# Performance work log

Measured on AMD Instinct MI355X. Metric: run time of the kernel, lower is better.

## Reference

```python
import jax, jax.numpy as jnp
import numpy as np

B, N, F = 8, 1024, 512
H, D = 4, 128  # num_heads, output_dim
LEAKY_ALPHA = 0.2
MASK_VAL = -1e10


def setup_inputs() -> dict:
    key = jax.random.key(0)
    ks = jax.random.split(key, 6)
    X = jax.random.normal(ks[0], (B, N, F), dtype=jnp.float32)
    A = (jax.random.uniform(ks[1], (B, N, N)) < 0.05).astype(jnp.float32)
    A = jnp.maximum(A, jnp.eye(N, dtype=jnp.float32)[None])
    W_att = jax.random.normal(ks[2], (H, F, D), dtype=jnp.float32) * (1.0 / np.sqrt(F))
    a_att = jax.random.normal(ks[3], (H, 2, D), dtype=jnp.float32) * (1.0 / np.sqrt(D))
    kernel = jax.random.normal(ks[4], (H, F, D), dtype=jnp.float32) * (1.0 / np.sqrt(F))
    bias = jax.random.normal(ks[5], (H * D,), dtype=jnp.float32) * 0.02
    return {"X": X, "A": A, "W_att": W_att, "a_att": a_att, "kernel": kernel, "bias": bias}


def reference(X, A, W_att, a_att, kernel, bias):
    # Per-head feature projection used only for attention scores: [H,B,N,D]
    xf = jnp.einsum('bnf,hfd->hbnd', X, W_att)
    att_self = jnp.einsum('hbnd,hd->hbn', xf, a_att[:, 0])       # [H,B,N]
    att_neigh = jnp.einsum('hbnd,hd->hbn', xf, a_att[:, 1])      # [H,B,N]
    # additive scores: scores[h,b,i,j] = self[i] + neigh[j]
    scores = att_self[..., :, None] + att_neigh[..., None, :]    # [H,B,N,N]
    scores = jnp.where(scores >= 0, scores, LEAKY_ALPHA * scores)
    scores = scores + MASK_VAL * (1.0 - A)[None]                 # adjacency mask
    attn = jax.nn.softmax(scores, axis=-1)                       # [H,B,N,N]
    # aggregate raw features X, then per-head kernel projection
    agg = jnp.einsum('hbij,bjf->hbif', attn, X)                  # [H,B,N,F]
    out = jnp.einsum('hbnf,hfd->bnhd', agg, kernel)              # [B,N,H,D]
    out = out.reshape(out.shape[0], out.shape[1], -1)            # concat heads -> [B,N,H*D]
    out = out + bias
    return jax.nn.elu(out)
```

## Files before the change

kernel.cpp:

```cpp
#include <hip/hip_runtime.h>
#include <hip/hip_bf16.h>
#include <math.h>

namespace {
constexpr int B = 8, N = 1024, F = 512, H = 4, D = 128, HD = H * D;
constexpr int ROWS = B * N;
constexpr float LEAKY = 0.2f;

constexpr size_t UV_OFF  = 0;
constexpr size_t ATT_OFF = 4096;
constexpr size_t Y_OFF   = 69632;
constexpr size_t XB_OFF  = 2166784;
constexpr size_t WKB_OFF = 4263936;
}

typedef __attribute__((ext_vector_type(8))) short short8;
typedef __attribute__((ext_vector_type(4))) float f32x4;

__device__ __forceinline__ ushort bf16bits(float x) {
    __hip_bfloat16 h = __float2bfloat16(x);
    return *reinterpret_cast<ushort*>(&h);
}
__device__ __forceinline__ float blo(uint u) {
    return __uint_as_float(u << 16);
}
__device__ __forceinline__ float bhi(uint u) {
    return __uint_as_float(u & 0xffff0000u);
}

extern "C" __global__ __launch_bounds__(256) void k_pre(
    const float* __restrict__ Watt, const float* __restrict__ aatt,
    const float* __restrict__ Wk, float* __restrict__ uv,
    __hip_bfloat16* __restrict__ Wkb) {
    __shared__ ushort T[128][136];
    if (blockIdx.x < 16) {
        int h = blockIdx.x >> 2, f0 = (blockIdx.x & 3) * 128;
#pragma unroll
        for (int p = 0; p < 16; ++p) {
            int fi = p * 8 + (threadIdx.x >> 5);
            int d4 = (threadIdx.x & 31) * 4;
            float4 v = *reinterpret_cast<const float4*>(
                Wk + ((size_t)h * F + f0 + fi) * D + d4);
            T[d4 + 0][fi] = bf16bits(v.x);
            T[d4 + 1][fi] = bf16bits(v.y);
            T[d4 + 2][fi] = bf16bits(v.z);
            T[d4 + 3][fi] = bf16bits(v.w);
        }
        __syncthreads();
        int d = threadIdx.x >> 1, hf = threadIdx.x & 1;
        ushort* dst =
            (ushort*)Wkb + (size_t)(h * 128 + d) * F + f0 + hf * 64;
        const ushort* src = &T[d][hf * 64];
#pragma unroll
        for (int q = 0; q < 8; ++q)
            *reinterpret_cast<uint4*>(dst + q * 8) =
                *reinterpret_cast<const uint4*>(src + q * 8);
    } else {
        int t = (blockIdx.x - 16) * 256 + threadIdx.x;
        int f = t % F;
        int h = (t / F) % H;
        int w = t / (F * H);
        const float* Wrow = Watt + (size_t)(h * F + f) * D;
        const float* arow = aatt + (size_t)(h * 2 + w) * D;
        float s = 0.f;
#pragma unroll 4
        for (int d = 0; d < D; ++d) s = fmaf(Wrow[d], arow[d], s);
        uv[(size_t)w * (H * F) + h * F + f] = s;
    }
}

extern "C" __global__ __launch_bounds__(256) void k_att(
    const float* __restrict__ X, const float* __restrict__ uv,
    float* __restrict__ att, __hip_bfloat16* __restrict__ Xb) {
    int wave = threadIdx.x >> 6, lane = threadIdx.x & 63;
    int row = blockIdx.x * 4 + wave;
    const float4* xr = reinterpret_cast<const float4*>(X + (size_t)row * F);
    float4 v0 = xr[lane * 2], v1 = xr[lane * 2 + 1];

    union { short8 s; ushort u[8]; } pk;
    pk.u[0] = bf16bits(v0.x); pk.u[1] = bf16bits(v0.y);
    pk.u[2] = bf16bits(v0.z); pk.u[3] = bf16bits(v0.w);
    pk.u[4] = bf16bits(v1.x); pk.u[5] = bf16bits(v1.y);
    pk.u[6] = bf16bits(v1.z); pk.u[7] = bf16bits(v1.w);
    *reinterpret_cast<short8*>(Xb + (size_t)row * F + lane * 8) = pk.s;

    float acc[2][H];
#pragma unroll
    for (int w = 0; w < 2; ++w)
#pragma unroll
        for (int h = 0; h < H; ++h) {
            const float4* up = reinterpret_cast<const float4*>(
                uv + (size_t)w * (H * F) + h * F + lane * 8);
            float4 u0 = up[0], u1 = up[1];
            float a = 0.f;
            a = fmaf(v0.x, u0.x, a); a = fmaf(v0.y, u0.y, a);
            a = fmaf(v0.z, u0.z, a); a = fmaf(v0.w, u0.w, a);
            a = fmaf(v1.x, u1.x, a); a = fmaf(v1.y, u1.y, a);
            a = fmaf(v1.z, u1.z, a); a = fmaf(v1.w, u1.w, a);
            acc[w][h] = a;
        }
#pragma unroll
    for (int w = 0; w < 2; ++w)
#pragma unroll
        for (int h = 0; h < H; ++h) {
            float v = acc[w][h];
#pragma unroll
            for (int off = 32; off > 0; off >>= 1) v += __shfl_xor(v, off);
            if (lane == 0) att[(size_t)w * (H * ROWS) + h * ROWS + row] = v;
        }
}

extern "C" __global__ __launch_bounds__(256) void k_gemm(
    const __hip_bfloat16* __restrict__ Xb,
    const __hip_bfloat16* __restrict__ Wkb,
    __hip_bfloat16* __restrict__ Y) {
    __shared__ __align__(16) char smem[24576];
    int tid = threadIdx.x;
    int lane = tid & 63, wv = tid >> 6;
    int wr = wv >> 1, wc = wv & 1;
    int lt = (blockIdx.x & 7) * 64 + (blockIdx.x >> 3);
    int bm = lt >> 3, bn = lt & 7;
    int row0 = bm * 128, col0 = bn * 64;

    const ushort* Ag = (const ushort*)Xb;
    const ushort* Bg = (const ushort*)Wkb;

    int aoff[4][2], boff[2][2];
#pragma unroll
    for (int ks = 0; ks < 2; ++ks) {
        int cb = ks * 4 + (lane >> 4);
#pragma unroll
        for (int mi = 0; mi < 4; ++mi) {
            int ra = wr * 64 + mi * 16 + (lane & 15);
            aoff[mi][ks] = ra * 128 + (cb ^ (ra & 7)) * 16;
        }
#pragma unroll
        for (int ni = 0; ni < 2; ++ni) {
            int rb = wc * 32 + ni * 16 + (lane & 15);
            boff[ni][ks] = 16384 + rb * 128 + (cb ^ (rb & 7)) * 16;
        }
    }
    int srowA[4], sgbA[4], srowB[2], sgbB[2];
#pragma unroll
    for (int i = 0; i < 4; ++i) {
        srowA[i] = i * 32 + wv * 8 + (lane >> 3);
        sgbA[i] = (lane & 7) ^ (srowA[i] & 7);
    }
#pragma unroll
    for (int i = 0; i < 2; ++i) {
        srowB[i] = i * 32 + wv * 8 + (lane >> 3);
        sgbB[i] = (lane & 7) ^ (srowB[i] & 7);
    }

    f32x4 acc[4][2] = {};
    for (int k0 = 0; k0 < F; k0 += 64) {
        __syncthreads();
#pragma unroll
        for (int i = 0; i < 4; ++i) {
            const ushort* ga = Ag + (size_t)(row0 + srowA[i]) * F + k0 + sgbA[i] * 8;
            __builtin_amdgcn_global_load_lds(
                (const __attribute__((address_space(1))) uint32_t*)ga,
                (__attribute__((address_space(3))) uint32_t*)(smem + i * 4096 + wv * 1024),
                16, 0, 0);
        }
#pragma unroll
        for (int i = 0; i < 2; ++i) {
            const ushort* gb = Bg + (size_t)(col0 + srowB[i]) * F + k0 + sgbB[i] * 8;
            __builtin_amdgcn_global_load_lds(
                (const __attribute__((address_space(1))) uint32_t*)gb,
                (__attribute__((address_space(3))) uint32_t*)(smem + 16384 + i * 4096 + wv * 1024),
                16, 0, 0);
        }
        __syncthreads();
#pragma unroll
        for (int ks = 0; ks < 2; ++ks) {
            short8 af[4], bf[2];
#pragma unroll
            for (int mi = 0; mi < 4; ++mi)
                af[mi] = *reinterpret_cast<short8*>(smem + aoff[mi][ks]);
#pragma unroll
            for (int ni = 0; ni < 2; ++ni)
                bf[ni] = *reinterpret_cast<short8*>(smem + boff[ni][ks]);
#pragma unroll
            for (int mi = 0; mi < 4; ++mi)
#pragma unroll
                for (int ni = 0; ni < 2; ++ni)
                    acc[mi][ni] = __builtin_amdgcn_mfma_f32_16x16x32_bf16(
                        af[mi], bf[ni], acc[mi][ni], 0, 0, 0);
        }
    }
    int cr = (lane >> 4) * 4, cc = lane & 15;
#pragma unroll
    for (int mi = 0; mi < 4; ++mi)
#pragma unroll
        for (int ni = 0; ni < 2; ++ni) {
            int gr = row0 + wr * 64 + mi * 16 + cr;
            int gc = col0 + wc * 32 + ni * 16 + cc;
#pragma unroll
            for (int r = 0; r < 4; ++r)
                Y[(size_t)(gr + r) * HD + gc] =
                    __float2bfloat16(acc[mi][ni][r]);
        }
}

extern "C" __global__ __launch_bounds__(256) void k_attn_agg(
    const float* __restrict__ A, const float* __restrict__ att,
    const ushort* __restrict__ Y, const float* __restrict__ bias,
    float* __restrict__ out) {
    int g = blockIdx.x;
    int bi = ((g & 7) << 10) | (g >> 3);
    int b = bi >> 10;
    int tid = threadIdx.x;
    int lane = tid & 63, wv = tid >> 6;
    __shared__ int idxs[N];
    __shared__ int2 ent[H][256];
    __shared__ int wsum[4];

    const float* Arow = A + (size_t)bi * N;
    float4 av = *reinterpret_cast<const float4*>(Arow + tid * 4);
    int cnt = (av.x != 0.f) + (av.y != 0.f) + (av.z != 0.f) + (av.w != 0.f);
    int isc = cnt;
#pragma unroll
    for (int off = 1; off < 64; off <<= 1) {
        int t = __shfl_up(isc, off);
        if (lane >= off) isc += t;
    }
    if (lane == 63) wsum[wv] = isc;
    __syncthreads();
    int prefix = 0;
#pragma unroll
    for (int wj = 0; wj < 4; ++wj) prefix += (wj < wv) ? wsum[wj] : 0;
    int nnz = wsum[0] + wsum[1] + wsum[2] + wsum[3];
    int wo = prefix + isc - cnt;
    int jb = tid * 4;
    if (av.x != 0.f) idxs[wo++] = jb;
    if (av.y != 0.f) idxs[wo++] = jb + 1;
    if (av.z != 0.f) idxs[wo++] = jb + 2;
    if (av.w != 0.f) idxs[wo++] = jb + 3;
    __syncthreads();

    int h = wv;
    int grp = lane >> 4, sub = lane & 15;
    float sself = att[(size_t)h * ROWS + bi];
    const float* nrow = att + (size_t)(H + h) * ROWS + (size_t)b * N;
    const char* Ybyte = (const char*)(Y + ((size_t)b * N) * HD + h * D + sub * 8);

    float m = -1e30f, l = 0.f;
    float acc[8] = {};
    for (int c0 = 0; c0 < nnz; c0 += 256) {
        int cn = min(256, nnz - c0);
        int kpad = (cn + 15) & ~15;
        float lm = -1e30f;
        for (int k = lane; k < cn; k += 64) {
            int idx = idxs[c0 + k];
            float s = sself + nrow[idx];
            s = s >= 0.f ? s : LEAKY * s;
            ent[h][k] = make_int2(idx << 10, __float_as_int(s));
            lm = fmaxf(lm, s);
        }
        for (int k = cn + lane; k < kpad; k += 64) ent[h][k] = make_int2(0, 0);
#pragma unroll
        for (int off = 32; off > 0; off >>= 1)
            lm = fmaxf(lm, __shfl_xor(lm, off));
        float mn = fmaxf(m, lm);
        float scale = __expf(m - mn);
        float ls = 0.f;
        for (int k = lane; k < cn; k += 64) {
            int2 p = ent[h][k];
            float e = __expf(__int_as_float(p.y) - mn);
            ent[h][k].y = __float_as_int(e);
            ls += e;
        }
#pragma unroll
        for (int off = 32; off > 0; off >>= 1) ls += __shfl_xor(ls, off);
        l = fmaf(l, scale, ls);
#pragma unroll
        for (int q = 0; q < 8; ++q) acc[q] *= scale;
        m = mn;
        for (int k = 0; k < kpad; k += 16) {
            int2 p[4];
#pragma unroll
            for (int q = 0; q < 4; ++q) p[q] = ent[h][k + q * 4 + grp];
            uint4 y[4];
#pragma unroll
            for (int q = 0; q < 4; ++q)
                y[q] = *reinterpret_cast<const uint4*>(Ybyte + (size_t)(uint)p[q].x);
#pragma unroll
            for (int q = 0; q < 4; ++q) {
                float w = __int_as_float(p[q].y);
                acc[0] = fmaf(w, blo(y[q].x), acc[0]);
                acc[1] = fmaf(w, bhi(y[q].x), acc[1]);
                acc[2] = fmaf(w, blo(y[q].y), acc[2]);
                acc[3] = fmaf(w, bhi(y[q].y), acc[3]);
                acc[4] = fmaf(w, blo(y[q].z), acc[4]);
                acc[5] = fmaf(w, bhi(y[q].z), acc[5]);
                acc[6] = fmaf(w, blo(y[q].w), acc[6]);
                acc[7] = fmaf(w, bhi(y[q].w), acc[7]);
            }
        }
    }
#pragma unroll
    for (int q = 0; q < 8; ++q) {
        acc[q] += __shfl_xor(acc[q], 16);
        acc[q] += __shfl_xor(acc[q], 32);
    }
    if (grp == 0) {
        float inv = 1.f / l;
        int cbase = h * D + sub * 8;
        float4 b0 = *reinterpret_cast<const float4*>(bias + cbase);
        float4 b1 = *reinterpret_cast<const float4*>(bias + cbase + 4);
        float o[8];
        o[0] = acc[0] * inv + b0.x; o[1] = acc[1] * inv + b0.y;
        o[2] = acc[2] * inv + b0.z; o[3] = acc[3] * inv + b0.w;
        o[4] = acc[4] * inv + b1.x; o[5] = acc[5] * inv + b1.y;
        o[6] = acc[6] * inv + b1.z; o[7] = acc[7] * inv + b1.w;
#pragma unroll
        for (int q = 0; q < 8; ++q)
            o[q] = o[q] > 0.f ? o[q] : (__expf(o[q]) - 1.f);
        float* op = out + (size_t)bi * HD + cbase;
        *reinterpret_cast<float4*>(op) = make_float4(o[0], o[1], o[2], o[3]);
        *reinterpret_cast<float4*>(op + 4) = make_float4(o[4], o[5], o[6], o[7]);
    }
}

extern "C" void kernel_launch(void* const* d_in, const int* in_sizes, int n_in,
                              void* d_out, int out_size, void* d_ws,
                              size_t ws_size, hipStream_t stream) {
    const float* X    = (const float*)d_in[0];
    const float* A    = (const float*)d_in[1];
    const float* Watt = (const float*)d_in[2];
    const float* aatt = (const float*)d_in[3];
    const float* Wk   = (const float*)d_in[4];
    const float* bias = (const float*)d_in[5];
    float* out = (float*)d_out;
    float* ws  = (float*)d_ws;

    float* uv  = ws + UV_OFF;
    float* att = ws + ATT_OFF;
    __hip_bfloat16* Yb  = (__hip_bfloat16*)(ws + Y_OFF);
    __hip_bfloat16* Xb  = (__hip_bfloat16*)(ws + XB_OFF);
    __hip_bfloat16* Wkb = (__hip_bfloat16*)(ws + WKB_OFF);

    hipLaunchKernelGGL(k_pre, dim3(32), dim3(256), 0, stream, Watt, aatt, Wk,
                       uv, Wkb);
    hipLaunchKernelGGL(k_att, dim3(ROWS / 4), dim3(256), 0, stream, X, uv, att, Xb);
    hipLaunchKernelGGL(k_gemm, dim3((ROWS / 128) * (HD / 64)), dim3(256), 0,
                       stream, Xb, Wkb, Yb);
    hipLaunchKernelGGL(k_attn_agg, dim3(ROWS), dim3(256), 0, stream, A, att,
                       (const ushort*)Yb, bias, out);
}
```

Baseline: 64.93 us.

## Use precomputed row-max bound for softmax and pass weights via shuffles

The online softmax with per-chunk max reductions and rescaling is replaced by a fixed upper bound, leaky(sself + max over the neighbour scores), computed once per wave. Because leaky ReLU is monotonic this bound is at least every score, so the exponentials stay at or below one. Per-chunk weights and indices now stay in registers and are broadcast with shuffles, which removes the shared-memory staging buffer and two reduction passes. The risk is underflow when the bound is far above the real masked-row maximum; with this data's score scale that is unlikely. The extra cost is reading the full 1024-entry neighbour row per wave.

Measured after the change: 66.81 us. 2.9% more time.

```diff
diff --git a/kernel.cpp b/kernel.cpp
--- a/kernel.cpp
+++ b/kernel.cpp
@@ -213,7 +213,6 @@
     int tid = threadIdx.x;
     int lane = tid & 63, wv = tid >> 6;
     __shared__ int idxs[N];
-    __shared__ int2 ent[H][256];
     __shared__ int wsum[4];
 
     const float* Arow = A + (size_t)bi * N;
@@ -241,71 +240,73 @@
 
     int h = wv;
     int grp = lane >> 4, sub = lane & 15;
+    const float* nrow = att + (size_t)(H + h) * ROWS + (size_t)b * N;
+
+    float nmax = -1e30f;
+    const float4* nr4 = reinterpret_cast<const float4*>(nrow);
+#pragma unroll
+    for (int q = 0; q < 4; ++q) {
+        float4 v = nr4[lane + q * 64];
+        nmax = fmaxf(fmaxf(nmax, fmaxf(v.x, v.y)), fmaxf(v.z, v.w));
+    }
+#pragma unroll
+    for (int off = 32; off > 0; off >>= 1)
+        nmax = fmaxf(nmax, __shfl_xor(nmax, off));
     float sself = att[(size_t)h * ROWS + bi];
-    const float* nrow = att + (size_t)(H + h) * ROWS + (size_t)b * N;
+    float m = sself + nmax;
+    m = fmaxf(m, LEAKY * m);
+
     const char* Ybyte = (const char*)(Y + ((size_t)b * N) * HD + h * D + sub * 8);
-
-    float m = -1e30f, l = 0.f;
+    float lsum = 0.f;
     float acc[8] = {};
-    for (int c0 = 0; c0 < nnz; c0 += 256) {
-        int cn = min(256, nnz - c0);
+    for (int c0 = 0; c0 < nnz; c0 += 64) {
+        int cn = min(64, nnz - c0);
+        int idx = 0;
+        float e = 0.f;
+        if (lane < cn) {
+            idx = idxs[c0 + lane];
+            float s = sself + nrow[idx];
+            s = fmaxf(s, LEAKY * s);
+            e = __expf(s - m);
+        }
+        lsum += e;
         int kpad = (cn + 15) & ~15;
-        float lm = -1e30f;
-        for (int k = lane; k < cn; k += 64) {
-            int idx = idxs[c0 + k];
-            float s = sself + nrow[idx];
-            s = s >= 0.f ? s : LEAKY * s;
-            ent[h][k] = make_int2(idx << 10, __float_as_int(s));
-            lm = fmaxf(lm, s);
-        }
-        for (int k = cn + lane; k < kpad; k += 64) ent[h][k] = make_int2(0, 0);
-#pragma unroll
-        for (int off = 32; off > 0; off >>= 1)
-            lm = fmaxf(lm, __shfl_xor(lm, off));
-        float mn = fmaxf(m, lm);
-        float scale = __expf(m - mn);
-        float ls = 0.f;
-        for (int k = lane; k < cn; k += 64) {
-            int2 p = ent[h][k];
-            float e = __expf(__int_as_float(p.y) - mn);
-            ent[h][k].y = __float_as_int(e);
-            ls += e;
-        }
-#pragma unroll
-        for (int off = 32; off > 0; off >>= 1) ls += __shfl_xor(ls, off);
-        l = fmaf(l, scale, ls);
-#pragma unroll
-        for (int q = 0; q < 8; ++q) acc[q] *= scale;
-        m = mn;
         for (int k = 0; k < kpad; k += 16) {
-            int2 p[4];
-#pragma unroll
-            for (int q = 0; q < 4; ++q) p[q] = ent[h][k + q * 4 + grp];
+            float w[4];
+            int off4[4];
+#pragma unroll
+            for (int q = 0; q < 4; ++q) {
+                int src = k + q * 4 + grp;
+                w[q] = __shfl(e, src);
+                off4[q] = __shfl(idx, src) << 10;
+            }
             uint4 y[4];
 #pragma unroll
             for (int q = 0; q < 4; ++q)
-                y[q] = *reinterpret_cast<const uint4*>(Ybyte + (size_t)(uint)p[q].x);
+                y[q] = *reinterpret_cast<const uint4*>(
+                    Ybyte + (size_t)(uint)off4[q]);
 #pragma unroll
             for (int q = 0; q < 4; ++q) {
-                float w = __int_as_float(p[q].y);
-                acc[0] = fmaf(w, blo(y[q].x), acc[0]);
-                acc[1] = fmaf(w, bhi(y[q].x), acc[1]);
-                acc[2] = fmaf(w, blo(y[q].y), acc[2]);
-                acc[3] = fmaf(w, bhi(y[q].y), acc[3]);
-                acc[4] = fmaf(w, blo(y[q].z), acc[4]);
-                acc[5] = fmaf(w, bhi(y[q].z), acc[5]);
-                acc[6] = fmaf(w, blo(y[q].w), acc[6]);
-                acc[7] = fmaf(w, bhi(y[q].w), acc[7]);
+                acc[0] = fmaf(w[q], blo(y[q].x), acc[0]);
+                acc[1] = fmaf(w[q], bhi(y[q].x), acc[1]);
+                acc[2] = fmaf(w[q], blo(y[q].y), acc[2]);
+                acc[3] = fmaf(w[q], bhi(y[q].y), acc[3]);
+                acc[4] = fmaf(w[q], blo(y[q].z), acc[4]);
+                acc[5] = fmaf(w[q], bhi(y[q].z), acc[5]);
+                acc[6] = fmaf(w[q], blo(y[q].w), acc[6]);
+                acc[7] = fmaf(w[q], bhi(y[q].w), acc[7]);
             }
         }
     }
+#pragma unroll
+    for (int off = 32; off > 0; off >>= 1) lsum += __shfl_xor(lsum, off);
 #pragma unroll
     for (int q = 0; q < 8; ++q) {
         acc[q] += __shfl_xor(acc[q], 16);
         acc[q] += __shfl_xor(acc[q], 32);
     }
     if (grp == 0) {
-        float inv = 1.f / l;
+        float inv = 1.f / lsum;
         int cbase = h * D + sub * 8;
         float4 b0 = *reinterpret_cast<const float4*>(bias + cbase);
         float4 b1 = *reinterpret_cast<const float4*>(bias + cbase + 4);
```
